# Optimization experiments

Hardware: AMD Instinct MI355X
Metric: run time of the kernel (lower is better)

The kernel has to match this reference:

```python
import jax, jax.numpy as jnp
import numpy as np

N_TASKS = 8
D_MODEL = 1024
HIDDEN = 1024
N_CLASSES = 100
BATCH = 8192


def setup_inputs() -> dict:
    key = jax.random.key(0)
    ks = jax.random.split(key, 6)
    s1 = 1.0 / np.sqrt(D_MODEL)
    s2 = 1.0 / np.sqrt(HIDDEN)
    return {
        "x": jax.random.normal(ks[0], (BATCH, D_MODEL), dtype=jnp.float32),
        "task_id": jax.random.randint(ks[1], (BATCH,), 0, N_TASKS),
        "W1": jax.random.uniform(ks[2], (N_TASKS, D_MODEL, HIDDEN), jnp.float32, -s1, s1),
        "b1": jax.random.uniform(ks[3], (N_TASKS, HIDDEN), jnp.float32, -s1, s1),
        "W2": jax.random.uniform(ks[4], (N_TASKS, HIDDEN, N_CLASSES), jnp.float32, -s2, s2),
        "b2": jax.random.uniform(ks[5], (N_TASKS, N_CLASSES), jnp.float32, -s2, s2),
    }


def reference(x, task_id, W1, b1, W2, b2):
    # Per-task 2-layer MLP heads; dropout is identity (inference).
    # Compute all heads batched, then select each row's head via one-hot.
    h = jax.nn.relu(jnp.einsum("bd,tdh->tbh", x, W1) + b1[:, None, :])  # [T,B,H]
    logits = jnp.einsum("tbh,thc->tbc", h, W2) + b2[:, None, :]          # [T,B,C]
    onehot = jax.nn.one_hot(task_id, W1.shape[0], dtype=x.dtype)          # [B,T]
    return jnp.einsum("tbc,bt->bc", logits, onehot)                      # [B,C]
```

## Files before the change

kernel.cpp:

```cpp
#include <hip/hip_runtime.h>
#include <hip/hip_bf16.h>
#include <stdint.h>

#define T_TASKS 8
#define DM      1024
#define HID     1024
#define NC      100
#define NCP     128
#define BATCH   8192
#define MPAD    9216

typedef __bf16 bf16x8 __attribute__((ext_vector_type(8)));
typedef float  f32x4  __attribute__((ext_vector_type(4)));
typedef unsigned int u32;
#define GAS __attribute__((address_space(1)))
#define LAS __attribute__((address_space(3)))

__device__ __forceinline__ unsigned short f2bf(float f) {
  __hip_bfloat16 h = __float2bfloat16(f);
  return __builtin_bit_cast(unsigned short, h);
}

__device__ __forceinline__ float bf2f(unsigned short u) {
  const u32 v = ((u32)u) << 16;
  return __builtin_bit_cast(float, v);
}

#define SORT_BLKS 32
#define W1_BLKS (T_TASKS * 16 * 16)
#define W2_BLKS (16 * T_TASKS)
__global__ void sortpre_k(const int* __restrict__ task_id,
                          const float* __restrict__ W1,
                          unsigned short* __restrict__ W1T,
                          const float* __restrict__ W2,
                          unsigned short* __restrict__ W2F,
                          int* __restrict__ perm, int* __restrict__ starts) {
  __shared__ __align__(16) unsigned short tile[128 * 72];
  __shared__ int sAux[25];
  const int bid = blockIdx.x;
  const int tid = threadIdx.x;

  if (bid < SORT_BLKS) {
    int* hist = (int*)tile;
    int* tot  = sAux;
    int* prev = sAux + 8;
    int* sst  = sAux + 16;
#pragma unroll
    for (int t = 0; t < T_TASKS; ++t) hist[tid * 8 + t] = 0;
    __syncthreads();
    const int cbase = tid * 32;
    for (int i = 0; i < 32; ++i) {
      const int t = task_id[cbase + i];
      hist[tid * 8 + t] += 1;
    }
    __syncthreads();
    if (tid < T_TASKS) {
      int s = 0;
      for (int r = 0; r < 256; ++r) s += hist[r * 8 + tid];
      tot[tid] = s;
    } else if (tid < 2 * T_TASKS) {
      const int t = tid - T_TASKS;
      const int lim = bid * 8;
      int s = 0;
      for (int r = 0; r < lim; ++r) s += hist[r * 8 + t];
      prev[t] = s;
    }
    __syncthreads();
    if (tid == 0) {
      int off = 0;
      for (int t = 0; t < T_TASKS; ++t) { sst[t] = off; off += (tot[t] + 127) & ~127; }
      sst[T_TASKS] = off;
    }
    if (tid < T_TASKS) hist[tid] = 0;
    __syncthreads();
    const int r = bid * 256 + tid;
    const int t = task_id[r];
    const int slot = atomicAdd(&hist[t], 1);
    perm[sst[t] + prev[t] + slot] = r;
    if (tid < 32) {
      const int g = bid * 32 + tid;
      int acc = 0, pos = -1;
#pragma unroll
      for (int t2 = 0; t2 < T_TASKS; ++t2) {
        const int pc = sst[t2 + 1] - sst[t2] - tot[t2];
        if (pos < 0 && g < acc + pc) pos = sst[t2] + tot[t2] + (g - acc);
        acc += pc;
      }
      if (pos < 0) pos = sst[T_TASKS] + (g - acc);
      perm[pos] = -1;
    }
    if (bid == 0 && tid <= T_TASKS) starts[tid] = sst[tid];
    return;
  }

  if (bid < SORT_BLKS + W1_BLKS) {
    const int b  = bid - SORT_BLKS;
    const int t  = b >> 8;
    const int rem = b & 255;
    const int d0 = (rem >> 4) * 64;
    const int h0 = (rem & 15) * 64;
    const float* src = W1 + (size_t)t * DM * HID;
    unsigned short* dst = W1T + (size_t)t * HID * DM;
#pragma unroll
    for (int i = 0; i < 4; ++i) {
      const int idx = tid + 256 * i;
      const int d  = idx >> 4;
      const int hc = (idx & 15) * 4;
      const float4 f = *(const float4*)(src + (size_t)(d0 + d) * HID + h0 + hc);
      tile[(hc + 0) * 65 + d] = f2bf(f.x);
      tile[(hc + 1) * 65 + d] = f2bf(f.y);
      tile[(hc + 2) * 65 + d] = f2bf(f.z);
      tile[(hc + 3) * 65 + d] = f2bf(f.w);
    }
    __syncthreads();
#pragma unroll
    for (int i = 0; i < 2; ++i) {
      const int idx = tid + 256 * i;
      const int lh  = idx >> 3;
      const int ldc = idx & 7;
      union { uint4 v; unsigned short s[8]; } o;
#pragma unroll
      for (int q = 0; q < 8; ++q) o.s[q] = tile[lh * 65 + ldc * 8 + q];
      *(uint4*)(dst + (size_t)(h0 + lh) * DM + d0 + ldc * 8) = o.v;
    }
    return;
  }

  {
    const int b  = bid - (SORT_BLKS + W1_BLKS);
    const int t  = b >> 4;
    const int h0 = (b & 15) * 64;
    const float* src = W2 + (size_t)t * HID * NC;
#pragma unroll
    for (int i = 0; i < 36; ++i) tile[tid + 256 * i] = 0;
    __syncthreads();
#pragma unroll
    for (int i = 0; i < 32; ++i) {
      const int idx = tid + 256 * i;
      const int row = idx >> 7, col = idx & 127;
      if (col < NC)
        tile[col * 72 + row] = f2bf(src[(size_t)(h0 + row) * NC + col]);
    }
    __syncthreads();
    const int w = tid >> 6, lane = tid & 63;
    const int lr = lane & 15, quad = lane >> 4;
#pragma unroll
    for (int e = 0; e < 4; ++e) {
      const int fi = w * 4 + e;
      const int ci = fi >> 1, kcl = fi & 1;
      const uint4 v = *(const uint4*)&tile[(ci * 16 + lr) * 72 + kcl * 32 + quad * 8];
      unsigned short* dstp =
          W2F + (((size_t)t * 8 + ci) * 32 + (h0 >> 5) + kcl) * 512 + lane * 8;
      *(uint4*)dstp = v;
    }
  }
}

__global__ void gather_k(const float* __restrict__ x,
                         const int* __restrict__ perm,
                         unsigned short* __restrict__ XP) {
  const int bid = blockIdx.x;
  const int tid = threadIdx.x;
  const int r = perm[bid];
  const int c = tid * 4;
  ushort4 v;
  if (r >= 0) {
    const float4 f = *(const float4*)(x + (size_t)r * DM + c);
    v.x = f2bf(f.x); v.y = f2bf(f.y); v.z = f2bf(f.z); v.w = f2bf(f.w);
  } else {
    v.x = 0; v.y = 0; v.z = 0; v.w = 0;
  }
  *(ushort4*)(XP + (size_t)bid * DM + c) = v;
}

__global__ __launch_bounds__(256, 3) void gemm_fused4(
    const unsigned short* __restrict__ XP,
    const unsigned short* __restrict__ W1T,
    const unsigned short* __restrict__ W2F,
    const float* __restrict__ b1,
    const int* __restrict__ starts,
    unsigned short* __restrict__ Lp)
{
  __shared__ __align__(16) unsigned short lds[18432];
  unsigned short* As = lds;
  unsigned short* Bs = lds + 8192;
  unsigned short* hS = lds;

  const int tid = threadIdx.x;

  const int L   = blockIdx.y * gridDim.x + blockIdx.x;
  const int xcd = L & 7;
  const int idx = L >> 3;
  const int bx  = xcd * 9 + (idx % 9);
  const int by  = idx / 9;

  const int p0  = bx * 128;
  const int n0  = by * 128;

  if (p0 >= starts[T_TASKS]) return;

  int task = 0;
#pragma unroll
  for (int t = 1; t < T_TASKS; ++t)
    if (p0 >= starts[t]) task = t;

  const int wave = tid >> 6;
  const int lane = tid & 63;
  const int wm   = (wave >> 1) * 64;
  const int wn   = (wave & 1) * 64;
  const int lr   = lane & 15;
  const int quad = lane >> 4;

  const int crow = tid >> 3;
  const int kc   = (tid & 7) ^ (crow & 7);
  const unsigned short* pA[4];
  const unsigned short* pB[4];
  const unsigned short* Bg = W1T + ((size_t)task * HID + n0) * 1024;
#pragma unroll
  for (int i = 0; i < 4; ++i) {
    const int row = crow + 32 * i;
    pA[i] = XP + (size_t)(p0 + row) * 1024 + kc * 8;
    pB[i] = Bg + (size_t)row * 1024 + kc * 8;
  }

  f32x4 acc[4][4];
#pragma unroll
  for (int i = 0; i < 4; ++i)
#pragma unroll
    for (int j = 0; j < 4; ++j) acc[i][j] = (f32x4){0.f, 0.f, 0.f, 0.f};

  const int sw0 = quad ^ (lr & 7);
  const int sw1 = (4 + quad) ^ (lr & 7);

  for (int k0 = 0; k0 < 1024; k0 += 64) {
#pragma unroll
    for (int i = 0; i < 4; ++i) {
      __builtin_amdgcn_global_load_lds((const GAS u32*)(pA[i] + k0),
                                       (LAS u32*)&As[(tid + 256 * i) * 8], 16, 0, 0);
      __builtin_amdgcn_global_load_lds((const GAS u32*)(pB[i] + k0),
                                       (LAS u32*)&Bs[(tid + 256 * i) * 8], 16, 0, 0);
    }
    __syncthreads();
    {
      bf16x8 a[4], b[4];
#pragma unroll
      for (int i = 0; i < 4; ++i)
        a[i] = *(const bf16x8*)&As[((wm + i * 16 + lr) * 8 + sw0) * 8];
#pragma unroll
      for (int j = 0; j < 4; ++j)
        b[j] = *(const bf16x8*)&Bs[((wn + j * 16 + lr) * 8 + sw0) * 8];
#pragma unroll
      for (int i = 0; i < 4; ++i)
#pragma unroll
        for (int j = 0; j < 4; ++j)
          acc[i][j] = __builtin_amdgcn_mfma_f32_16x16x32_bf16(a[i], b[j], acc[i][j], 0, 0, 0);
#pragma unroll
      for (int i = 0; i < 4; ++i)
        a[i] = *(const bf16x8*)&As[((wm + i * 16 + lr) * 8 + sw1) * 8];
#pragma unroll
      for (int j = 0; j < 4; ++j)
        b[j] = *(const bf16x8*)&Bs[((wn + j * 16 + lr) * 8 + sw1) * 8];
#pragma unroll
      for (int i = 0; i < 4; ++i)
#pragma unroll
        for (int j = 0; j < 4; ++j)
          acc[i][j] = __builtin_amdgcn_mfma_f32_16x16x32_bf16(a[i], b[j], acc[i][j], 0, 0, 0);
    }
    __syncthreads();
  }

  float b1v[4];
#pragma unroll
  for (int ni = 0; ni < 4; ++ni)
    b1v[ni] = b1[task * HID + n0 + wn + ni * 16 + lr];
#pragma unroll
  for (int mi = 0; mi < 4; ++mi)
#pragma unroll
    for (int r = 0; r < 4; ++r) {
      const int row = wm + mi * 16 + quad * 4 + r;
#pragma unroll
      for (int ni = 0; ni < 4; ++ni) {
        float v = acc[mi][ni][r] + b1v[ni];
        v = v > 0.f ? v : 0.f;
        hS[row * 136 + wn + ni * 16 + lr] = f2bf(v);
      }
    }
  __syncthreads();

  const int cbase = (wave & 1) * 4;
  const unsigned short* pW2 =
      W2F + (((size_t)task * 8 + cbase) * 32 + by * 4) * 512 + lane * 8;

  f32x4 acc2[4][4];
#pragma unroll
  for (int mi = 0; mi < 4; ++mi)
#pragma unroll
    for (int ci = 0; ci < 4; ++ci) acc2[mi][ci] = (f32x4){0.f, 0.f, 0.f, 0.f};

#pragma unroll
  for (int e = 0; e < 4; ++e) {
    bf16x8 w2p[4], a2[4];
#pragma unroll
    for (int ci = 0; ci < 4; ++ci)
      w2p[ci] = *(const bf16x8*)(pW2 + ((size_t)ci * 32 + e) * 512);
#pragma unroll
    for (int mi = 0; mi < 4; ++mi)
      a2[mi] = *(const bf16x8*)&hS[(wm + mi * 16 + lr) * 136 + e * 32 + quad * 8];
#pragma unroll
    for (int mi = 0; mi < 4; ++mi)
#pragma unroll
      for (int ci = 0; ci < 4; ++ci)
        acc2[mi][ci] = __builtin_amdgcn_mfma_f32_16x16x32_bf16(
            a2[mi], w2p[ci], acc2[mi][ci], 0, 0, 0);
  }

  unsigned short* lp = Lp + ((size_t)by * MPAD + p0) * NCP;
#pragma unroll
  for (int mi = 0; mi < 4; ++mi)
#pragma unroll
    for (int r = 0; r < 4; ++r) {
      const int row = wm + mi * 16 + quad * 4 + r;
#pragma unroll
      for (int ci = 0; ci < 4; ++ci) {
        if (wn + ci * 16 < NC)
          lp[row * NCP + wn + ci * 16 + lr] = f2bf(acc2[mi][ci][r]);
      }
    }
}

__global__ void reduce_k(const unsigned short* __restrict__ Lp,
                         const int* __restrict__ perm,
                         const int* __restrict__ task_id,
                         const float* __restrict__ b2,
                         float* __restrict__ Out) {
  const int gid = blockIdx.x * 256 + threadIdx.x;
  const int row = gid >> 5;
  const int c4  = (gid & 31) * 4;
  if (c4 >= NC) return;
  const int og = perm[row];
  if (og < 0) return;
  float s0 = 0.f, s1 = 0.f, s2 = 0.f, s3 = 0.f;
#pragma unroll
  for (int sp = 0; sp < 8; ++sp) {
    const ushort4 v = *(const ushort4*)(Lp + ((size_t)sp * MPAD + row) * NCP + c4);
    s0 += bf2f(v.x); s1 += bf2f(v.y); s2 += bf2f(v.z); s3 += bf2f(v.w);
  }
  const int task = task_id[og];
  const float4 bb = *(const float4*)(b2 + (size_t)task * NC + c4);
  float4 o;
  o.x = s0 + bb.x; o.y = s1 + bb.y; o.z = s2 + bb.z; o.w = s3 + bb.w;
  *(float4*)(Out + (size_t)og * NC + c4) = o;
}

extern "C" void kernel_launch(void* const* d_in, const int* in_sizes, int n_in,
                              void* d_out, int out_size, void* d_ws, size_t ws_size,
                              hipStream_t stream) {
  const float* x       = (const float*)d_in[0];
  const int*   task_id = (const int*)d_in[1];
  const float* W1      = (const float*)d_in[2];
  const float* b1      = (const float*)d_in[3];
  const float* W2      = (const float*)d_in[4];
  const float* b2      = (const float*)d_in[5];
  float* out = (float*)d_out;

  char* ws = (char*)d_ws;
  int* perm   = (int*)(ws + 0);
  int* starts = (int*)(ws + 37888);
  unsigned short* XP  = (unsigned short*)(ws + 65536);
  unsigned short* W1T = (unsigned short*)(ws + 18939904);
  unsigned short* W2F = (unsigned short*)(ws + 35717120);
  unsigned short* Lp  = (unsigned short*)(ws + 37814272);

  sortpre_k<<<SORT_BLKS + W1_BLKS + W2_BLKS, 256, 0, stream>>>(
      task_id, W1, W1T, W2, W2F, perm, starts);
  gather_k<<<MPAD, 256, 0, stream>>>(x, perm, XP);
  gemm_fused4<<<dim3(MPAD / 128, HID / 128), 256, 0, stream>>>(
      XP, W1T, W2F, b1, starts, Lp);
  reduce_k<<<MPAD * 32 / 256, 256, 0, stream>>>(Lp, perm, task_id, b2, out);
}
```

Measured before the change: 147.4 us.

## Fold x bf16 conversion into preprocessing kernel and gather rows inside GEMM

```diff
diff --git a/kernel.cpp b/kernel.cpp
--- a/kernel.cpp
+++ b/kernel.cpp
@@ -29,11 +29,15 @@
 #define SORT_BLKS 32
 #define W1_BLKS (T_TASKS * 16 * 16)
 #define W2_BLKS (16 * T_TASKS)
+#define XB_BLKS (BATCH / 8)
 __global__ void sortpre_k(const int* __restrict__ task_id,
+                          const float* __restrict__ x,
                           const float* __restrict__ W1,
                           unsigned short* __restrict__ W1T,
                           const float* __restrict__ W2,
                           unsigned short* __restrict__ W2F,
+                          unsigned short* __restrict__ XB,
+                          unsigned short* __restrict__ zrow,
                           int* __restrict__ perm, int* __restrict__ starts) {
   __shared__ __align__(16) unsigned short tile[128 * 72];
   __shared__ int sAux[25];
@@ -45,6 +49,10 @@
     int* tot  = sAux;
     int* prev = sAux + 8;
     int* sst  = sAux + 16;
+    if (bid == 0) {
+      ushort4 z; z.x = 0; z.y = 0; z.z = 0; z.w = 0;
+      *(ushort4*)(zrow + tid * 4) = z;
+    }
 #pragma unroll
     for (int t = 0; t < T_TASKS; ++t) hist[tid * 8 + t] = 0;
     __syncthreads();
@@ -126,7 +134,7 @@
     return;
   }
 
-  {
+  if (bid < SORT_BLKS + W1_BLKS + W2_BLKS) {
     const int b  = bid - (SORT_BLKS + W1_BLKS);
     const int t  = b >> 4;
     const int h0 = (b & 15) * 64;
@@ -153,32 +161,34 @@
           W2F + (((size_t)t * 8 + ci) * 32 + (h0 >> 5) + kcl) * 512 + lane * 8;
       *(uint4*)dstp = v;
     }
-  }
-}
-
-__global__ void gather_k(const float* __restrict__ x,
-                         const int* __restrict__ perm,
-                         unsigned short* __restrict__ XP) {
-  const int bid = blockIdx.x;
-  const int tid = threadIdx.x;
-  const int r = perm[bid];
-  const int c = tid * 4;
-  ushort4 v;
-  if (r >= 0) {
-    const float4 f = *(const float4*)(x + (size_t)r * DM + c);
-    v.x = f2bf(f.x); v.y = f2bf(f.y); v.z = f2bf(f.z); v.w = f2bf(f.w);
-  } else {
-    v.x = 0; v.y = 0; v.z = 0; v.w = 0;
-  }
-  *(ushort4*)(XP + (size_t)bid * DM + c) = v;
+    return;
+  }
+
+  {
+    const int b   = bid - (SORT_BLKS + W1_BLKS + W2_BLKS);
+    const int row = b * 8 + (tid >> 5);
+    const int l   = (tid & 31) * 4;
+    const float* src = x + (size_t)row * DM;
+    unsigned short* dst = XB + (size_t)row * DM;
+#pragma unroll
+    for (int j = 0; j < 8; ++j) {
+      const int c = l + j * 128;
+      const float4 f = *(const float4*)(src + c);
+      ushort4 v;
+      v.x = f2bf(f.x); v.y = f2bf(f.y); v.z = f2bf(f.z); v.w = f2bf(f.w);
+      *(ushort4*)(dst + c) = v;
+    }
+  }
 }
 
 __global__ __launch_bounds__(256, 3) void gemm_fused4(
-    const unsigned short* __restrict__ XP,
+    const unsigned short* __restrict__ XB,
     const unsigned short* __restrict__ W1T,
     const unsigned short* __restrict__ W2F,
     const float* __restrict__ b1,
     const int* __restrict__ starts,
+    const int* __restrict__ perm,
+    const unsigned short* __restrict__ zrow,
     unsigned short* __restrict__ Lp)
 {
   __shared__ __align__(16) unsigned short lds[18432];
@@ -219,7 +229,9 @@
 #pragma unroll
   for (int i = 0; i < 4; ++i) {
     const int row = crow + 32 * i;
-    pA[i] = XP + (size_t)(p0 + row) * 1024 + kc * 8;
+    const int og  = perm[p0 + row];
+    const unsigned short* base = (og >= 0) ? (XB + (size_t)og * 1024) : zrow;
+    pA[i] = base + kc * 8;
     pB[i] = Bg + (size_t)row * 1024 + kc * 8;
   }
 
@@ -366,15 +378,15 @@
   char* ws = (char*)d_ws;
   int* perm   = (int*)(ws + 0);
   int* starts = (int*)(ws + 37888);
-  unsigned short* XP  = (unsigned short*)(ws + 65536);
+  unsigned short* zrow = (unsigned short*)(ws + 40960);
+  unsigned short* XB  = (unsigned short*)(ws + 65536);
   unsigned short* W1T = (unsigned short*)(ws + 18939904);
   unsigned short* W2F = (unsigned short*)(ws + 35717120);
   unsigned short* Lp  = (unsigned short*)(ws + 37814272);
 
-  sortpre_k<<<SORT_BLKS + W1_BLKS + W2_BLKS, 256, 0, stream>>>(
-      task_id, W1, W1T, W2, W2F, perm, starts);
-  gather_k<<<MPAD, 256, 0, stream>>>(x, perm, XP);
+  sortpre_k<<<SORT_BLKS + W1_BLKS + W2_BLKS + XB_BLKS, 256, 0, stream>>>(
+      task_id, x, W1, W1T, W2, W2F, XB, zrow, perm, starts);
   gemm_fused4<<<dim3(MPAD / 128, HID / 128), 256, 0, stream>>>(
-      XP, W1T, W2F, b1, starts, Lp);
+      XB, W1T, W2F, b1, starts, perm, zrow, Lp);
   reduce_k<<<MPAD * 32 / 256, 256, 0, stream>>>(Lp, perm, task_id, b2, out);
 }
```

Result: faster. 142.2 us (-3.5%).
